# Performance work log

Hardware: AMD Instinct MI355X
Metric: run time of the kernel (lower is better)

## Reference

```python
import jax, jax.numpy as jnp
import numpy as np

EPS = 1e-10


def setup_inputs() -> dict:
    key = jax.random.key(0)
    ks = jax.random.split(key, 8)
    N, C, H, W = 32, 512, 14, 14
    D, HID = 2048, 256
    s1 = 1.0 / np.sqrt(C + D)
    s2 = 1.0 / np.sqrt(HID)
    return {
        "local_feature": jax.random.normal(ks[0], (N, C, H, W), jnp.float32),
        "global_feature": jax.random.normal(ks[1], (N, D, 1, 1), jnp.float32),
        "W1": jax.random.normal(ks[2], (C + D, HID), jnp.float32) * s1,
        "b1": jnp.zeros((HID,), jnp.float32),
        "W2": jax.random.normal(ks[3], (HID, HID), jnp.float32) * s2,
        "b2": jnp.zeros((HID,), jnp.float32),
        "W3": jax.random.normal(ks[4], (HID, 1), jnp.float32) * s2,
        "b3": jnp.zeros((1,), jnp.float32),
    }


def reference(local_feature, global_feature, W1, b1, W2, b2, W3, b3):
    # Vectorized form of DMIEstimator.calculate_mi (the per-sample Python loop
    # collapsed into one batched pass with a block-diagonal negative mask).
    N, C, H, W = local_feature.shape
    hw = H * W
    nhw = N * hw
    D = global_feature.shape[1]

    lf = jnp.transpose(local_feature, (0, 2, 3, 1)).reshape(nhw, C)   # [nhw, C]
    gf = global_feature[:, :, 0, 0]                                   # [N, D]

    # combined = cat([global, local], -1); split the first Linear accordingly
    # so the [N*nhw, C+D] concat tensor is never materialized.
    h_loc = lf @ W1[D:]                        # [nhw, HID]
    h_glb = gf @ W1[:D] + b1                   # [N, HID]
    h1 = jax.nn.relu(h_glb[:, None, :] + h_loc[None, :, :])  # [N, nhw, HID]
    h2 = jax.nn.relu(h1 @ W2 + b2)                            # [N, nhw, HID]
    scores = (h2 @ W3)[..., 0] + b3[0]                        # [N, nhw]

    mx = jnp.max(scores, axis=1, keepdims=True)               # [N, 1]
    ex = jnp.exp(scores - mx)

    # negatives for sample i exclude its own hw block [hw*i, hw*(i+1))
    own = (jnp.arange(nhw)[None, :] // hw) == jnp.arange(N)[:, None]  # [N, nhw]
    neg_mean = jnp.where(own, 0.0, ex).sum(axis=1) / (nhw - hw) + EPS  # [N]

    # positive (diagonal) block of scores: scores[i, hw*i : hw*(i+1)]
    pos = scores.reshape(N, N, hw)[jnp.arange(N), jnp.arange(N)]       # [N, hw]

    mi = pos - mx - jnp.log(neg_mean)[:, None]                         # [N, hw]
    return mi.reshape(N, H, W)
```

## Files before the change

### kernel.cpp

```cpp
#include <hip/hip_runtime.h>
#include <math.h>

#define NB   32
#define CC   512
#define DD   2048
#define HWP  196
#define NHW  6272
#define HID  256

typedef _Float16 h8 __attribute__((ext_vector_type(8)));
typedef _Float16 h4 __attribute__((ext_vector_type(4)));
typedef float    f4 __attribute__((ext_vector_type(4)));
union F4H8 { f4 f; h8 h; };

__device__ __forceinline__ int fragIdx(int j, int k) {
    return ((j >> 6) << 14) + (((k >> 5) * 4 + ((j & 63) >> 4)) << 9)
         + (((((k >> 3) & 3) << 4) + (j & 15)) << 3) + (k & 7);
}

__global__ __launch_bounds__(256) void prep_kernel(const float* __restrict__ lf,
                                                   const float* __restrict__ gf,
                                                   const float* __restrict__ W1,
                                                   const float* __restrict__ W2,
                                                   float* __restrict__ hpart,
                                                   _Float16* __restrict__ W2F,
                                                   _Float16* __restrict__ W1F,
                                                   _Float16* __restrict__ lf16T) {
    int bid = blockIdx.x, tid = threadIdx.x;
    if (bid < 512) {
        int i = bid >> 4, ky = bid & 15, k = tid;
        const float* g = gf + (size_t)i * DD + ky * 128;
        const float* w = W1 + (size_t)(ky * 128) * HID + k;
        float acc = 0.f;
        #pragma unroll 8
        for (int r = 0; r < 128; r++) acc = fmaf(g[r], w[(size_t)r * HID], acc);
        hpart[((size_t)i * 16 + ky) * HID + k] = acc;
    } else if (bid < 608) {
        int tg = (bid - 512) * 256 + tid;
        if (tg < 8192) {
            int t = tg, F = t >> 6, l = t & 63;
            int k2t = F >> 3, ks = F & 7;
            int kb = ks * 32 + (l >> 4) * 8;
            int n  = k2t * 16 + (l & 15);
            _Float16* o = W2F + (size_t)t * 8;
            #pragma unroll
            for (int j = 0; j < 8; j++) o[j] = (_Float16)W2[(size_t)(kb + j) * HID + n];
        } else {
            int t = tg - 8192, F = t >> 6, l = t & 63;
            int k2t = F >> 4, ks = F & 15;
            int kb = ks * 32 + (l >> 4) * 8;
            int n  = k2t * 16 + (l & 15);
            const float* W1c = W1 + (size_t)DD * HID;
            _Float16* o = W1F + (size_t)t * 8;
            #pragma unroll
            for (int j = 0; j < 8; j++) o[j] = (_Float16)W1c[(size_t)(kb + j) * HID + n];
        }
    } else {
        __shared__ _Float16 sT[64][HWP + 4];
        int b = bid - 608;
        int n = b >> 3, c0 = (b & 7) * 64;
        for (int task = tid; task < 64 * 49; task += 256) {
            int c = task / 49, f = task - c * 49;
            f4 v = *(const f4*)&lf[((size_t)n * CC + c0 + c) * HWP + f * 4];
            h4 o = { (_Float16)v.x, (_Float16)v.y, (_Float16)v.z, (_Float16)v.w };
            *(h4*)&sT[c][f * 4] = o;
        }
        __syncthreads();
        for (int task = tid; task < 8 * HWP; task += 256) {
            int ch = task / HWP, p = task - ch * HWP;
            h8 o;
            #pragma unroll
            for (int cc = 0; cc < 8; cc++) o[cc] = sT[ch * 8 + cc][p];
            *(h8*)&lf16T[((size_t)(n * HWP + p)) * CC + c0 + ch * 8] = o;
        }
    }
}

__global__ __launch_bounds__(256, 2) void hlocF_kernel(const _Float16* __restrict__ lf16T,
                                                       const _Float16* __restrict__ W1F,
                                                       const float* __restrict__ hpart,
                                                       const float* __restrict__ b1,
                                                       _Float16* __restrict__ g16,
                                                       _Float16* __restrict__ hF) {
    if (blockIdx.x == 196) {
        int kh = blockIdx.y;
        for (int x = threadIdx.x; x < 16 * HID; x += 256) {
            int i = kh * 16 + (x >> 8), k = x & 255;
            float s = b1[k];
            #pragma unroll
            for (int ky = 0; ky < 16; ky++) s += hpart[((size_t)i * 16 + ky) * HID + k];
            g16[(size_t)i * HID + k] = (_Float16)s;
        }
        return;
    }
    __shared__ _Float16 sLf[32][CC + 16];
    int tid = threadIdx.x;
    int w = tid >> 6, l = tid & 63, quad = l >> 4, ln = l & 15;
    int j0 = blockIdx.x * 32;
    int khalf = blockIdx.y;

    #pragma unroll
    for (int s = 0; s < 8; s++) {
        int y = s * 256 + tid;
        int row = y >> 6, col = (y & 63) * 8;
        h8 v = *(const h8*)&lf16T[(size_t)(j0 + row) * CC + col];
        *(h8*)&sLf[row][col] = v;
    }

    F4H8 Af[32];
    {
        const f4* src = (const f4*)W1F + l;
        #pragma unroll
        for (int mt = 0; mt < 2; mt++)
            #pragma unroll
            for (int ks = 0; ks < 16; ks++)
                Af[mt * 16 + ks].f = src[(size_t)((khalf * 8 + w * 2 + mt) * 16 + ks) * 64];
    }
    __syncthreads();

    f4 acc[4] = {};
    #pragma unroll
    for (int ks = 0; ks < 16; ks++) {
        h8 bF[2];
        #pragma unroll
        for (int nt = 0; nt < 2; nt++)
            bF[nt] = *(const h8*)&sLf[nt * 16 + ln][ks * 32 + quad * 8];
        #pragma unroll
        for (int mt = 0; mt < 2; mt++)
            #pragma unroll
            for (int nt = 0; nt < 2; nt++)
                acc[mt * 2 + nt] = __builtin_amdgcn_mfma_f32_16x16x32_f16(Af[mt * 16 + ks].h, bF[nt], acc[mt * 2 + nt], 0, 0, 0);
    }

    #pragma unroll
    for (int mt = 0; mt < 2; mt++)
        #pragma unroll
        for (int nt = 0; nt < 2; nt++)
            #pragma unroll
            for (int r = 0; r < 4; r++) {
                int j  = j0 + nt * 16 + ln;
                int k2 = khalf * 128 + w * 32 + mt * 16 + quad * 4 + r;
                hF[fragIdx(j, k2)] = (_Float16)acc[mt * 2 + nt][r];
            }
}

__global__ __launch_bounds__(512, 4) void score_kernel(const _Float16* __restrict__ hF,
                                                       const _Float16* __restrict__ g16,
                                                       const _Float16* __restrict__ W2F,
                                                       const float* __restrict__ b2,
                                                       const float* __restrict__ W3,
                                                       const float* __restrict__ b3,
                                                       float* __restrict__ scores) {
    __shared__ _Float16 sA[64 * HID];
    __shared__ float sRed[64][8];
    int tid = threadIdx.x, w = tid >> 6, l = tid & 63, quad = l >> 4, ln = l & 15;
    int bid = blockIdx.x;
    int i = bid & 31, jg = bid >> 5;

    F4H8 Af[16];
    {
        const f4* src = (const f4*)W2F + l;
        #pragma unroll
        for (int mt = 0; mt < 2; mt++)
            #pragma unroll
            for (int ks = 0; ks < 8; ks++)
                Af[mt * 8 + ks].f = src[(size_t)((w * 2 + mt) * 8 + ks) * 64];
    }
    const _Float16* gbase = g16 + (size_t)i * HID;
    float bias3 = b3[0];

    #pragma unroll 1
    for (int t = 0; t < 2; t++) {
        int jt = jg * 2 + t;

        {
            const _Float16* hbase = hF + (size_t)jt * 16384;
            h8 z = {};
            #pragma unroll
            for (int s = 0; s < 4; s++) {
                int y = s * 512 + tid;
                h8 hv = *(const h8*)&hbase[y * 8];
                h8 gq = *(const h8*)&gbase[(y >> 8) * 32 + ((y >> 4) & 3) * 8];
                h8 hz = __builtin_elementwise_max(hv + gq, z);
                *(h8*)&sA[y * 8] = hz;
            }
        }
        __syncthreads();

        #pragma unroll 1
        for (int pass = 0; pass < 2; pass++) {
            f4 acc[4];
            #pragma unroll
            for (int mt = 0; mt < 2; mt++) {
                f4 bv = *(const f4*)&b2[w * 32 + mt * 16 + quad * 4];
                #pragma unroll
                for (int nt = 0; nt < 2; nt++) acc[mt * 2 + nt] = bv;
            }
            #pragma unroll
            for (int ks = 0; ks < 8; ks++) {
                #pragma unroll
                for (int nt = 0; nt < 2; nt++) {
                    int ntg = pass * 2 + nt;
                    h8 hz = *(const h8*)&sA[(ks * 4 + ntg) * 512 + l * 8];
                    #pragma unroll
                    for (int mt = 0; mt < 2; mt++)
                        acc[mt * 2 + nt] = __builtin_amdgcn_mfma_f32_16x16x32_f16(Af[mt * 8 + ks].h, hz, acc[mt * 2 + nt], 0, 0, 0);
                }
            }
            #pragma unroll
            for (int nt = 0; nt < 2; nt++) {
                float s = 0.f;
                #pragma unroll
                for (int mt = 0; mt < 2; mt++) {
                    f4 w3v = *(const f4*)&W3[w * 32 + mt * 16 + quad * 4];
                    s += fmaxf(acc[mt * 2 + nt][0], 0.f) * w3v.x
                       + fmaxf(acc[mt * 2 + nt][1], 0.f) * w3v.y
                       + fmaxf(acc[mt * 2 + nt][2], 0.f) * w3v.z
                       + fmaxf(acc[mt * 2 + nt][3], 0.f) * w3v.w;
                }
                s += __shfl_xor(s, 16, 64);
                s += __shfl_xor(s, 32, 64);
                if (quad == 0) sRed[(pass * 2 + nt) * 16 + ln][w] = s;
            }
        }
        __syncthreads();
        if (tid < 64) {
            f4 a = *(const f4*)&sRed[tid][0];
            f4 b = *(const f4*)&sRed[tid][4];
            scores[(size_t)i * NHW + jt * 64 + tid] =
                a.x + a.y + a.z + a.w + b.x + b.y + b.z + b.w + bias3;
        }
    }
}

__global__ __launch_bounds__(1024) void reduce_kernel(const float* __restrict__ scores,
                                                      float* __restrict__ out) {
    int i = blockIdx.x, tid = threadIdx.x;
    const float* row = scores + (size_t)i * NHW;
    const f4* row4 = (const f4*)row;
    __shared__ float sW[16], sW2[16], sval[2];
    float mx = -1e30f;
    for (int q = tid; q < 1568; q += 1024) {
        f4 v = row4[q];
        mx = fmaxf(mx, fmaxf(fmaxf(v.x, v.y), fmaxf(v.z, v.w)));
    }
    #pragma unroll
    for (int off = 32; off > 0; off >>= 1) mx = fmaxf(mx, __shfl_down(mx, off, 64));
    if ((tid & 63) == 0) sW[tid >> 6] = mx;
    __syncthreads();
    if (tid == 0) {
        float m = sW[0];
        for (int c = 1; c < 16; c++) m = fmaxf(m, sW[c]);
        sval[0] = m;
    }
    __syncthreads();
    mx = sval[0];
    int q0 = i * 49, q1 = q0 + 49;
    float tot = 0.f, ownv = 0.f;
    for (int q = tid; q < 1568; q += 1024) {
        f4 v = row4[q];
        float e = expf(v.x - mx) + expf(v.y - mx) + expf(v.z - mx) + expf(v.w - mx);
        tot += e;
        if (q >= q0 && q < q1) ownv += e;
    }
    #pragma unroll
    for (int off = 32; off > 0; off >>= 1) {
        tot  += __shfl_down(tot, off, 64);
        ownv += __shfl_down(ownv, off, 64);
    }
    if ((tid & 63) == 0) { sW[tid >> 6] = tot; sW2[tid >> 6] = ownv; }
    __syncthreads();
    if (tid == 0) {
        float t = 0.f, o = 0.f;
        for (int c = 0; c < 16; c++) { t += sW[c]; o += sW2[c]; }
        float neg_mean = (t - o) / (float)(NHW - HWP) + 1e-10f;
        sval[1] = mx + logf(neg_mean);
    }
    __syncthreads();
    float sub = sval[1];
    if (tid < HWP) out[(size_t)i * HWP + tid] = row[i * HWP + tid] - sub;
}

extern "C" void kernel_launch(void* const* d_in, const int* in_sizes, int n_in,
                              void* d_out, int out_size, void* d_ws, size_t ws_size,
                              hipStream_t stream) {
    const float* lf = (const float*)d_in[0];
    const float* gf = (const float*)d_in[1];
    const float* W1 = (const float*)d_in[2];
    const float* b1 = (const float*)d_in[3];
    const float* W2 = (const float*)d_in[4];
    const float* b2 = (const float*)d_in[5];
    const float* W3 = (const float*)d_in[6];
    const float* b3 = (const float*)d_in[7];
    float* out = (float*)d_out;

    char* ws = (char*)d_ws;
    _Float16* hF     = (_Float16*)ws;
    _Float16* g16    = (_Float16*)(ws + 3211264);
    _Float16* W2F    = (_Float16*)(ws + 3227648);
    _Float16* W1F    = (_Float16*)(ws + 3358720);
    _Float16* lf16T  = (_Float16*)(ws + 3620864);
    float*    scores = (float*)   (ws + 10043392);
    float*    hpart  = (float*)   (ws + 10846208);

    hipLaunchKernelGGL(prep_kernel, dim3(864), dim3(256), 0, stream,
                       lf, gf, W1, W2, hpart, W2F, W1F, lf16T);
    hipLaunchKernelGGL(hlocF_kernel, dim3(197, 2), dim3(256), 0, stream,
                       lf16T, W1F, hpart, b1, g16, hF);
    hipLaunchKernelGGL(score_kernel, dim3(1568), dim3(512), 0, stream,
                       hF, g16, W2F, b2, W3, b3, scores);
    hipLaunchKernelGGL(reduce_kernel, dim3(NB), dim3(1024), 0, stream, scores, out);
}
```

Measured before the change: 129.3 us.

## Reuse staged hidden tile across four samples and reduce scores with atomics

The score kernel now stages each 64-row hloc tile into LDS once as raw fp16. It reuses that tile for four global samples, adding the per-sample global bias and ReLU in registers just before each MFMA, where before it restaged the tile for every sample. The cross-wave reduction through shared memory and the second barrier are replaced by global float atomicAdds into a scores buffer, which extra blocks in the prep kernel zero beforehand. The b3 bias is dropped, since the final MI output does not depend on a constant shift of the scores. The trade-off is redundant per-wave add/max work on the operands and many global atomics in place of one store per score.

```diff
diff --git a/kernel.cpp b/kernel.cpp
--- a/kernel.cpp
+++ b/kernel.cpp
@@ -25,7 +25,8 @@
                                                    float* __restrict__ hpart,
                                                    _Float16* __restrict__ W2F,
                                                    _Float16* __restrict__ W1F,
-                                                   _Float16* __restrict__ lf16T) {
+                                                   _Float16* __restrict__ lf16T,
+                                                   float* __restrict__ scores) {
     int bid = blockIdx.x, tid = threadIdx.x;
     if (bid < 512) {
         int i = bid >> 4, ky = bid & 15, k = tid;
@@ -55,7 +56,7 @@
             #pragma unroll
             for (int j = 0; j < 8; j++) o[j] = (_Float16)W1c[(size_t)(kb + j) * HID + n];
         }
-    } else {
+    } else if (bid < 864) {
         __shared__ _Float16 sT[64][HWP + 4];
         int b = bid - 608;
         int n = b >> 3, c0 = (b & 7) * 64;
@@ -73,6 +74,11 @@
             for (int cc = 0; cc < 8; cc++) o[cc] = sT[ch * 8 + cc][p];
             *(h8*)&lf16T[((size_t)(n * HWP + p)) * CC + c0 + ch * 8] = o;
         }
+    } else {
+        f4* sc4 = (f4*)scores;
+        int idx = (bid - 864) * 256 + tid;
+        f4 z = {};
+        for (int q = idx; q < NB * NHW / 4; q += 16384) sc4[q] = z;
     }
 }
 
@@ -149,13 +155,11 @@
                                                        const _Float16* __restrict__ W2F,
                                                        const float* __restrict__ b2,
                                                        const float* __restrict__ W3,
-                                                       const float* __restrict__ b3,
                                                        float* __restrict__ scores) {
     __shared__ _Float16 sA[64 * HID];
-    __shared__ float sRed[64][8];
     int tid = threadIdx.x, w = tid >> 6, l = tid & 63, quad = l >> 4, ln = l & 15;
     int bid = blockIdx.x;
-    int i = bid & 31, jg = bid >> 5;
+    int jt = bid >> 3, ib = bid & 7;
 
     F4H8 Af[16];
     {
@@ -166,69 +170,60 @@
             for (int ks = 0; ks < 8; ks++)
                 Af[mt * 8 + ks].f = src[(size_t)((w * 2 + mt) * 8 + ks) * 64];
     }
-    const _Float16* gbase = g16 + (size_t)i * HID;
-    float bias3 = b3[0];
+
+    {
+        const _Float16* hbase = hF + (size_t)jt * 16384;
+        #pragma unroll
+        for (int s = 0; s < 4; s++) {
+            int y = s * 512 + tid;
+            *(h8*)&sA[y * 8] = *(const h8*)&hbase[y * 8];
+        }
+    }
+    __syncthreads();
+
+    f4 b2v0 = *(const f4*)&b2[w * 32 + quad * 4];
+    f4 b2v1 = *(const f4*)&b2[w * 32 + 16 + quad * 4];
+    f4 w3v0 = *(const f4*)&W3[w * 32 + quad * 4];
+    f4 w3v1 = *(const f4*)&W3[w * 32 + 16 + quad * 4];
 
     #pragma unroll 1
-    for (int t = 0; t < 2; t++) {
-        int jt = jg * 2 + t;
-
-        {
-            const _Float16* hbase = hF + (size_t)jt * 16384;
-            h8 z = {};
-            #pragma unroll
-            for (int s = 0; s < 4; s++) {
-                int y = s * 512 + tid;
-                h8 hv = *(const h8*)&hbase[y * 8];
-                h8 gq = *(const h8*)&gbase[(y >> 8) * 32 + ((y >> 4) & 3) * 8];
-                h8 hz = __builtin_elementwise_max(hv + gq, z);
-                *(h8*)&sA[y * 8] = hz;
-            }
-        }
-        __syncthreads();
+    for (int ii = 0; ii < 4; ii++) {
+        int i = ib * 4 + ii;
+        const _Float16* gbase = g16 + (size_t)i * HID + quad * 8;
 
         #pragma unroll 1
         for (int pass = 0; pass < 2; pass++) {
             f4 acc[4];
-            #pragma unroll
-            for (int mt = 0; mt < 2; mt++) {
-                f4 bv = *(const f4*)&b2[w * 32 + mt * 16 + quad * 4];
-                #pragma unroll
-                for (int nt = 0; nt < 2; nt++) acc[mt * 2 + nt] = bv;
-            }
+            acc[0] = b2v0; acc[1] = b2v0;
+            acc[2] = b2v1; acc[3] = b2v1;
             #pragma unroll
             for (int ks = 0; ks < 8; ks++) {
+                h8 gq = *(const h8*)(gbase + ks * 32);
+                h8 z = {};
                 #pragma unroll
                 for (int nt = 0; nt < 2; nt++) {
                     int ntg = pass * 2 + nt;
-                    h8 hz = *(const h8*)&sA[(ks * 4 + ntg) * 512 + l * 8];
-                    #pragma unroll
-                    for (int mt = 0; mt < 2; mt++)
-                        acc[mt * 2 + nt] = __builtin_amdgcn_mfma_f32_16x16x32_f16(Af[mt * 8 + ks].h, hz, acc[mt * 2 + nt], 0, 0, 0);
+                    h8 hv = *(const h8*)&sA[(ks * 4 + ntg) * 512 + l * 8];
+                    h8 hz = __builtin_elementwise_max(hv + gq, z);
+                    acc[0 + nt] = __builtin_amdgcn_mfma_f32_16x16x32_f16(Af[ks].h,     hz, acc[0 + nt], 0, 0, 0);
+                    acc[2 + nt] = __builtin_amdgcn_mfma_f32_16x16x32_f16(Af[8 + ks].h, hz, acc[2 + nt], 0, 0, 0);
                 }
             }
             #pragma unroll
             for (int nt = 0; nt < 2; nt++) {
-                float s = 0.f;
-                #pragma unroll
-                for (int mt = 0; mt < 2; mt++) {
-                    f4 w3v = *(const f4*)&W3[w * 32 + mt * 16 + quad * 4];
-                    s += fmaxf(acc[mt * 2 + nt][0], 0.f) * w3v.x
-                       + fmaxf(acc[mt * 2 + nt][1], 0.f) * w3v.y
-                       + fmaxf(acc[mt * 2 + nt][2], 0.f) * w3v.z
-                       + fmaxf(acc[mt * 2 + nt][3], 0.f) * w3v.w;
-                }
+                float s = fmaxf(acc[nt][0], 0.f) * w3v0.x
+                        + fmaxf(acc[nt][1], 0.f) * w3v0.y
+                        + fmaxf(acc[nt][2], 0.f) * w3v0.z
+                        + fmaxf(acc[nt][3], 0.f) * w3v0.w
+                        + fmaxf(acc[2 + nt][0], 0.f) * w3v1.x
+                        + fmaxf(acc[2 + nt][1], 0.f) * w3v1.y
+                        + fmaxf(acc[2 + nt][2], 0.f) * w3v1.z
+                        + fmaxf(acc[2 + nt][3], 0.f) * w3v1.w;
                 s += __shfl_xor(s, 16, 64);
                 s += __shfl_xor(s, 32, 64);
-                if (quad == 0) sRed[(pass * 2 + nt) * 16 + ln][w] = s;
+                if (quad == 0)
+                    atomicAdd(&scores[(size_t)i * NHW + jt * 64 + (pass * 2 + nt) * 16 + ln], s);
             }
-        }
-        __syncthreads();
-        if (tid < 64) {
-            f4 a = *(const f4*)&sRed[tid][0];
-            f4 b = *(const f4*)&sRed[tid][4];
-            scores[(size_t)i * NHW + jt * 64 + tid] =
-                a.x + a.y + a.z + a.w + b.x + b.y + b.z + b.w + bias3;
         }
     }
 }
@@ -291,7 +286,6 @@
     const float* W2 = (const float*)d_in[4];
     const float* b2 = (const float*)d_in[5];
     const float* W3 = (const float*)d_in[6];
-    const float* b3 = (const float*)d_in[7];
     float* out = (float*)d_out;
 
     char* ws = (char*)d_ws;
@@ -303,11 +297,11 @@
     float*    scores = (float*)   (ws + 10043392);
     float*    hpart  = (float*)   (ws + 10846208);
 
-    hipLaunchKernelGGL(prep_kernel, dim3(864), dim3(256), 0, stream,
-                       lf, gf, W1, W2, hpart, W2F, W1F, lf16T);
+    hipLaunchKernelGGL(prep_kernel, dim3(928), dim3(256), 0, stream,
+                       lf, gf, W1, W2, hpart, W2F, W1F, lf16T, scores);
     hipLaunchKernelGGL(hlocF_kernel, dim3(197, 2), dim3(256), 0, stream,
                        lf16T, W1F, hpart, b1, g16, hF);
-    hipLaunchKernelGGL(score_kernel, dim3(1568), dim3(512), 0, stream,
-                       hF, g16, W2F, b2, W3, b3, scores);
+    hipLaunchKernelGGL(score_kernel, dim3(784), dim3(512), 0, stream,
+                       hF, g16, W2F, b2, W3, scores);
     hipLaunchKernelGGL(reduce_kernel, dim3(NB), dim3(1024), 0, stream, scores, out);
 }
```

Result: slower. 178.8 us (+38.2%).
